# Kernel tuning notes

Measured on AMD Instinct MI355X. Metric: run time of the kernel, lower is better.

The kernel has to match this reference:

```python
import jax, jax.numpy as jnp
import numpy as np

NA, NB = 50000, 50000   # nodes of type A and B
E = 400000              # edges per canonical etype
D = 128                 # embed_size


def setup_inputs() -> dict:
    key = jax.random.key(0)
    ks = jax.random.split(key, 12)
    emb = lambda k, n: jax.random.normal(k, (n, D), dtype=jnp.float32) * 0.05
    return {
        "embed_r0": emb(ks[0], NA),       # srctype A for etype r0 (A->B)
        "embed_r1": emb(ks[1], NB),       # srctype B for etype r1 (B->A)
        "embed_r2": emb(ks[2], NA),       # srctype A for etype r2 (A->A)
        "self_embed_A": emb(ks[3], NA),
        "self_embed_B": emb(ks[4], NB),
        "h_bias": jnp.zeros((D,), jnp.float32),
        "src0": jax.random.randint(ks[5], (E,), 0, NA, dtype=jnp.int32),
        "dst0": jax.random.randint(ks[6], (E,), 0, NB, dtype=jnp.int32),
        "src1": jax.random.randint(ks[7], (E,), 0, NB, dtype=jnp.int32),
        "dst1": jax.random.randint(ks[8], (E,), 0, NA, dtype=jnp.int32),
        "src2": jax.random.randint(ks[9], (E,), 0, NA, dtype=jnp.int32),
        "dst2": jax.random.randint(ks[10], (E,), 0, NA, dtype=jnp.int32),
    }


def _mean_agg(embed, src, dst, n_dst):
    # DGL copy_u + mean: gather source embeds along edges, mean per dst node
    msg = embed[src]                                                   # [E, D]
    summed = jax.ops.segment_sum(msg, dst, num_segments=n_dst)         # [n_dst, D]
    cnt = jax.ops.segment_sum(jnp.ones((src.shape[0],), embed.dtype), dst,
                              num_segments=n_dst)                      # [n_dst]
    return summed / jnp.maximum(cnt, 1.0)[:, None]  # zero-indegree nodes -> 0


def reference(embed_r0, embed_r1, embed_r2, self_embed_A, self_embed_B, h_bias,
              src0, dst0, src1, dst1, src2, dst2):
    # multi_update_all(funcs, 'sum'): per-etype mean, then sum over etypes per dst ntype
    h_B = _mean_agg(embed_r0, src0, dst0, NB)
    h_A = _mean_agg(embed_r1, src1, dst1, NA) + _mean_agg(embed_r2, src2, dst2, NA)
    # fused epilogue: self-loop embed add, bias, activation; dropout p=0 -> identity
    h_A = jax.nn.relu(h_A + self_embed_A + h_bias)
    h_B = jax.nn.relu(h_B + self_embed_B + h_bias)
    return (h_A, h_B)
```

## Files before the change

kernel.cpp:

```cpp
#include <hip/hip_runtime.h>

#define D 128
#define SLOTS 32

typedef float vf4 __attribute__((ext_vector_type(4)));
typedef int   vi2 __attribute__((ext_vector_type(2)));
typedef _Float16 half4 __attribute__((ext_vector_type(4)));
typedef _Float16 half8 __attribute__((ext_vector_type(8)));

__device__ __forceinline__ vf4 nt_load4(const float* p) {
    return __builtin_nontemporal_load(reinterpret_cast<const vf4*>(p));
}
__device__ __forceinline__ void nt_store4(float* p, vf4 v) {
    __builtin_nontemporal_store(v, reinterpret_cast<vf4*>(p));
}
__device__ __forceinline__ vf4 ld4(const float* p) {
    return *reinterpret_cast<const vf4*>(p);
}

__global__ void init_kernel(int* __restrict__ cnt, int nt, int clearBlocks,
                            const float* __restrict__ er1, const float* __restrict__ er2,
                            const float* __restrict__ er0,
                            _Float16* __restrict__ hdst,
                            long long s1, long long s2, long long s0) {
    if (blockIdx.x < clearBlocks) {
        int i = blockIdx.x * blockDim.x + threadIdx.x;
        if (i < nt) cnt[i] = 0;
        return;
    }
    long long t = (long long)(blockIdx.x - clearBlocks) * blockDim.x + threadIdx.x;
    long long f = t * 8;
    long long total = s1 + s2 + s0;
    if (f >= total) return;
    const float* sp; long long off;
    if (f < s1)           { sp = er1; off = f; }
    else if (f < s1 + s2) { sp = er2; off = f - s1; }
    else                  { sp = er0; off = f - s1 - s2; }
    vf4 a = nt_load4(sp + off);
    vf4 b = nt_load4(sp + off + 4);
    half8 h;
    h[0] = (_Float16)a.x; h[1] = (_Float16)a.y; h[2] = (_Float16)a.z; h[3] = (_Float16)a.w;
    h[4] = (_Float16)b.x; h[5] = (_Float16)b.y; h[6] = (_Float16)b.z; h[7] = (_Float16)b.w;
    __builtin_nontemporal_store(h, reinterpret_cast<half8*>(hdst + f));
}

__global__ void build_kernel(const int* __restrict__ src1, const int* __restrict__ dst1, int e1,
                             const int* __restrict__ src2, const int* __restrict__ dst2, int e2,
                             const int* __restrict__ src0, const int* __restrict__ dst0, int e0,
                             int* __restrict__ cnt, unsigned short* __restrict__ slots, int na) {
    int mypart = blockIdx.x & 7;
    int t = (blockIdx.x >> 3) * blockDim.x + threadIdx.x;
    int s, c;
    if (t < e1) {
        s = src1[t];
        c = 2 * dst1[t];
    } else if (t < e1 + e2) {
        int i = t - e1;
        s = src2[i];
        c = 2 * dst2[i] + 1;
    } else if (t < e1 + e2 + e0) {
        int i = t - e1 - e2;
        s = src0[i];
        c = 2 * na + dst0[i];
    } else return;
    if (((c >> 11) & 7) != mypart) return;
    int pos = atomicAdd(&cnt[c], 1);
    if (pos < SLOTS) slots[(size_t)c * SLOTS + pos] = (unsigned short)s;
}


template <bool F16>
__device__ __forceinline__ vf4 ldrow(const void* base, int idx, int col) {
    if constexpr (F16) {
        const _Float16* p = (const _Float16*)base + (size_t)idx * D + col;
        half4 h = *reinterpret_cast<const half4*>(p);
        vf4 r;
        r.x = (float)h[0]; r.y = (float)h[1]; r.z = (float)h[2]; r.w = (float)h[3];
        return r;
    } else {
        return ld4((const float*)base + (size_t)idx * D + col);
    }
}

template <bool F16>
__device__ __forceinline__ void seg_tail(const void* __restrict__ emb,
                                         int idxv, int j, int c, int col, vf4& acc) {
    for (; j + 3 < c; j += 4) {
        int i0 = __shfl(idxv, j + 0, 32), i1 = __shfl(idxv, j + 1, 32);
        int i2 = __shfl(idxv, j + 2, 32), i3 = __shfl(idxv, j + 3, 32);
        vf4 v0 = ldrow<F16>(emb, i0, col);
        vf4 v1 = ldrow<F16>(emb, i1, col);
        vf4 v2 = ldrow<F16>(emb, i2, col);
        vf4 v3 = ldrow<F16>(emb, i3, col);
        acc += (v0 + v1) + (v2 + v3);
    }
    for (; j < c; j++) {
        int s = __shfl(idxv, j, 32);
        acc += ldrow<F16>(emb, s, col);
    }
}

template <bool F16>
__device__ __forceinline__ void seg_dual(const void* __restrict__ ea, int idxa, int ca,
                                         const void* __restrict__ eb, int idxb, int cb,
                                         int col, vf4& sa, vf4& sb) {
    int j = 0;
    int m = (ca < cb) ? ca : cb;
    for (; j + 7 < m; j += 8) {
        int a0 = __shfl(idxa, j + 0, 32), a1 = __shfl(idxa, j + 1, 32);
        int a2 = __shfl(idxa, j + 2, 32), a3 = __shfl(idxa, j + 3, 32);
        int a4 = __shfl(idxa, j + 4, 32), a5 = __shfl(idxa, j + 5, 32);
        int a6 = __shfl(idxa, j + 6, 32), a7 = __shfl(idxa, j + 7, 32);
        int b0 = __shfl(idxb, j + 0, 32), b1 = __shfl(idxb, j + 1, 32);
        int b2 = __shfl(idxb, j + 2, 32), b3 = __shfl(idxb, j + 3, 32);
        int b4 = __shfl(idxb, j + 4, 32), b5 = __shfl(idxb, j + 5, 32);
        int b6 = __shfl(idxb, j + 6, 32), b7 = __shfl(idxb, j + 7, 32);
        vf4 va0 = ldrow<F16>(ea, a0, col);
        vf4 va1 = ldrow<F16>(ea, a1, col);
        vf4 va2 = ldrow<F16>(ea, a2, col);
        vf4 va3 = ldrow<F16>(ea, a3, col);
        vf4 va4 = ldrow<F16>(ea, a4, col);
        vf4 va5 = ldrow<F16>(ea, a5, col);
        vf4 va6 = ldrow<F16>(ea, a6, col);
        vf4 va7 = ldrow<F16>(ea, a7, col);
        vf4 vb0 = ldrow<F16>(eb, b0, col);
        vf4 vb1 = ldrow<F16>(eb, b1, col);
        vf4 vb2 = ldrow<F16>(eb, b2, col);
        vf4 vb3 = ldrow<F16>(eb, b3, col);
        vf4 vb4 = ldrow<F16>(eb, b4, col);
        vf4 vb5 = ldrow<F16>(eb, b5, col);
        vf4 vb6 = ldrow<F16>(eb, b6, col);
        vf4 vb7 = ldrow<F16>(eb, b7, col);
        sa += ((va0 + va1) + (va2 + va3)) + ((va4 + va5) + (va6 + va7));
        sb += ((vb0 + vb1) + (vb2 + vb3)) + ((vb4 + vb5) + (vb6 + vb7));
    }
    for (; j + 3 < m; j += 4) {
        int a0 = __shfl(idxa, j + 0, 32), a1 = __shfl(idxa, j + 1, 32);
        int a2 = __shfl(idxa, j + 2, 32), a3 = __shfl(idxa, j + 3, 32);
        int b0 = __shfl(idxb, j + 0, 32), b1 = __shfl(idxb, j + 1, 32);
        int b2 = __shfl(idxb, j + 2, 32), b3 = __shfl(idxb, j + 3, 32);
        vf4 va0 = ldrow<F16>(ea, a0, col);
        vf4 va1 = ldrow<F16>(ea, a1, col);
        vf4 va2 = ldrow<F16>(ea, a2, col);
        vf4 va3 = ldrow<F16>(ea, a3, col);
        vf4 vb0 = ldrow<F16>(eb, b0, col);
        vf4 vb1 = ldrow<F16>(eb, b1, col);
        vf4 vb2 = ldrow<F16>(eb, b2, col);
        vf4 vb3 = ldrow<F16>(eb, b3, col);
        sa += (va0 + va1) + (va2 + va3);
        sb += (vb0 + vb1) + (vb2 + vb3);
    }
    seg_tail<F16>(ea, idxa, j, ca, col, sa);
    seg_tail<F16>(eb, idxb, j, cb, col, sb);
}

__device__ __forceinline__ vf4 relu4(vf4 v) {
    v.x = fmaxf(v.x, 0.0f); v.y = fmaxf(v.y, 0.0f);
    v.z = fmaxf(v.z, 0.0f); v.w = fmaxf(v.w, 0.0f);
    return v;
}

template <bool F16>
__global__ void gather_kernel(const void* __restrict__ emb1,
                              const void* __restrict__ emb2,
                              const void* __restrict__ emb0,
                              const unsigned short* __restrict__ slots,
                              const int* __restrict__ cnt,
                              const float* __restrict__ selfA,
                              const float* __restrict__ selfB,
                              const float* __restrict__ bias,
                              float* __restrict__ out,
                              int na, int nb) {
    int tid = blockIdx.x * blockDim.x + threadIdx.x;
    int gid = tid >> 5;
    int lane = tid & 31;
    int col = lane * 4;
    int nbg = (nb + 1) >> 1;
    if (gid >= na + nbg) return;
    vf4 b = ld4(bias + col);
    if (gid < na) {
        int r = gid;
        vi2 cc = __builtin_nontemporal_load(reinterpret_cast<const vi2*>(cnt + 2 * r));
        int c1 = min(cc.x, SLOTS);
        int c2 = min(cc.y, SLOTS);
        int idx1 = (lane < c1)
            ? (int)__builtin_nontemporal_load(slots + (size_t)(2 * r) * SLOTS + lane) : 0;
        int idx2 = (lane < c2)
            ? (int)__builtin_nontemporal_load(slots + (size_t)(2 * r + 1) * SLOTS + lane) : 0;
        vf4 s1 = {0.f, 0.f, 0.f, 0.f}, s2 = {0.f, 0.f, 0.f, 0.f};
        seg_dual<F16>(emb1, idx1, c1, emb2, idx2, c2, col, s1, s2);
        float inv1 = (c1 > 0) ? 1.0f / (float)c1 : 0.0f;
        float inv2 = (c2 > 0) ? 1.0f / (float)c2 : 0.0f;
        vf4 sf = nt_load4(selfA + (size_t)r * D + col);
        vf4 rr = relu4(s1 * inv1 + s2 * inv2 + sf + b);
        nt_store4(out + (size_t)r * D + col, rr);
    } else {
        int g = gid - na;
        int ra = 2 * g, rb = 2 * g + 1;
        bool hasB = rb < nb;
        vi2 cc = __builtin_nontemporal_load(
            reinterpret_cast<const vi2*>(cnt + 2 * na + ra));
        int ca = min(cc.x, SLOTS);
        int cb = hasB ? min(cc.y, SLOTS) : 0;
        int idxa = (lane < ca)
            ? (int)__builtin_nontemporal_load(slots + (size_t)(2 * na + ra) * SLOTS + lane) : 0;
        int idxb = (lane < cb)
            ? (int)__builtin_nontemporal_load(slots + (size_t)(2 * na + rb) * SLOTS + lane) : 0;
        vf4 sa = {0.f, 0.f, 0.f, 0.f}, sb = {0.f, 0.f, 0.f, 0.f};
        seg_dual<F16>(emb0, idxa, ca, emb0, idxb, cb, col, sa, sb);
        float inva = (ca > 0) ? 1.0f / (float)ca : 0.0f;
        vf4 sfa = nt_load4(selfB + (size_t)ra * D + col);
        vf4 rra = relu4(sa * inva + sfa + b);
        nt_store4(out + (size_t)(na + ra) * D + col, rra);
        if (hasB) {
            float invb = (cb > 0) ? 1.0f / (float)cb : 0.0f;
            vf4 sfb = nt_load4(selfB + (size_t)rb * D + col);
            vf4 rrb = relu4(sb * invb + sfb + b);
            nt_store4(out + (size_t)(na + rb) * D + col, rrb);
        }
    }
}

extern "C" void kernel_launch(void* const* d_in, const int* in_sizes, int n_in,
                              void* d_out, int out_size, void* d_ws, size_t ws_size,
                              hipStream_t stream) {
    const float* embed_r0 = (const float*)d_in[0];
    const float* embed_r1 = (const float*)d_in[1];
    const float* embed_r2 = (const float*)d_in[2];
    const float* selfA    = (const float*)d_in[3];
    const float* selfB    = (const float*)d_in[4];
    const float* bias     = (const float*)d_in[5];
    const int*   src0     = (const int*)d_in[6];
    const int*   dst0     = (const int*)d_in[7];
    const int*   src1     = (const int*)d_in[8];
    const int*   dst1     = (const int*)d_in[9];
    const int*   src2     = (const int*)d_in[10];
    const int*   dst2     = (const int*)d_in[11];

    const int na = in_sizes[3] / D;
    const int nb = in_sizes[4] / D;
    const int e0 = in_sizes[6];
    const int e1 = in_sizes[8];
    const int e2 = in_sizes[10];
    const int etot = e0 + e1 + e2;
    const int NT = 2 * na + nb;

    float* out = (float*)d_out;

    char* ws   = (char*)d_ws;
    int* cnt   = (int*)ws;
    unsigned short* slots = (unsigned short*)(cnt + NT);
    size_t slotsBytes = (size_t)NT * SLOTS * sizeof(unsigned short);
    _Float16* h16 = (_Float16*)((char*)slots + slotsBytes);

    const long long s1 = (long long)nb * D;
    const long long s2 = (long long)na * D;
    const long long s0 = (long long)na * D;
    const long long cvtN = s1 + s2 + s0;
    size_t needed = (size_t)NT * sizeof(int) + slotsBytes + (size_t)cvtN * sizeof(_Float16);
    const bool useF16 = ws_size >= needed;

    const int T = 256;

    int clearBlocks = (NT + T - 1) / T;
    int cvtBlocks = useF16 ? (int)((cvtN / 8 + T - 1) / T) : 0;
    init_kernel<<<clearBlocks + cvtBlocks, T, 0, stream>>>(
        cnt, NT, clearBlocks, embed_r1, embed_r2, embed_r0, h16, s1, s2, s0);

    int nchunks = (etot + T - 1) / T;
    build_kernel<<<nchunks * 8, T, 0, stream>>>(
        src1, dst1, e1, src2, dst2, e2, src0, dst0, e0, cnt, slots, na);

    int nbg = (nb + 1) >> 1;
    int rows = na + nbg;
    long long gthreads = (long long)rows * 32;
    int gb = (int)((gthreads + T - 1) / T);
    if (useF16) {
        gather_kernel<true><<<gb, T, 0, stream>>>(h16, h16 + s1, h16 + s1 + s2, slots, cnt,
                                                  selfA, selfB, bias, out, na, nb);
    } else {
        gather_kernel<false><<<gb, T, 0, stream>>>(embed_r1, embed_r2, embed_r0, slots, cnt,
                                                   selfA, selfB, bias, out, na, nb);
    }
}
```

Before: 288.4 us.

## Match gather block-to-row mapping to build partitions and use cached metadata loads

The gather kernel now maps blocks so that each of the 8 partitions (blockIdx & 7) handles row stripes of 1024 groups. This mirrors the build kernel's partitioning of counters and slots by (c>>11)&7, presumably so that each XCD reads slot and count data that its own L2 already holds from the build phase. The nontemporal loads on cnt and slots become normal cached loads to exploit that locality, and the build kernel now loads the src index only after the partition filter, skipping reads it would discard. The striped mapping launches some blocks that return immediately and relies on the hardware assigning blocks to XCDs round-robin.

```diff
diff --git a/kernel.cpp b/kernel.cpp
--- a/kernel.cpp
+++ b/kernel.cpp
@@ -50,20 +50,22 @@
                              int* __restrict__ cnt, unsigned short* __restrict__ slots, int na) {
     int mypart = blockIdx.x & 7;
     int t = (blockIdx.x >> 3) * blockDim.x + threadIdx.x;
-    int s, c;
+    const int* __restrict__ sp;
+    int c;
     if (t < e1) {
-        s = src1[t];
         c = 2 * dst1[t];
+        sp = src1 + t;
     } else if (t < e1 + e2) {
         int i = t - e1;
-        s = src2[i];
         c = 2 * dst2[i] + 1;
+        sp = src2 + i;
     } else if (t < e1 + e2 + e0) {
         int i = t - e1 - e2;
-        s = src0[i];
         c = 2 * na + dst0[i];
+        sp = src0 + i;
     } else return;
     if (((c >> 11) & 7) != mypart) return;
+    int s = *sp;
     int pos = atomicAdd(&cnt[c], 1);
     if (pos < SLOTS) slots[(size_t)c * SLOTS + pos] = (unsigned short)s;
 }
@@ -171,22 +173,23 @@
                               const float* __restrict__ bias,
                               float* __restrict__ out,
                               int na, int nb) {
-    int tid = blockIdx.x * blockDim.x + threadIdx.x;
-    int gid = tid >> 5;
-    int lane = tid & 31;
+    int q = blockIdx.x & 7;
+    int idx = (blockIdx.x >> 3) * (blockDim.x >> 5) + (threadIdx.x >> 5);
+    int stripe = idx >> 10;
+    int within = idx & 1023;
+    int gid = (((stripe << 3) + q) << 10) + within;
+    int lane = threadIdx.x & 31;
     int col = lane * 4;
     int nbg = (nb + 1) >> 1;
     if (gid >= na + nbg) return;
     vf4 b = ld4(bias + col);
     if (gid < na) {
         int r = gid;
-        vi2 cc = __builtin_nontemporal_load(reinterpret_cast<const vi2*>(cnt + 2 * r));
+        vi2 cc = *reinterpret_cast<const vi2*>(cnt + 2 * r);
         int c1 = min(cc.x, SLOTS);
         int c2 = min(cc.y, SLOTS);
-        int idx1 = (lane < c1)
-            ? (int)__builtin_nontemporal_load(slots + (size_t)(2 * r) * SLOTS + lane) : 0;
-        int idx2 = (lane < c2)
-            ? (int)__builtin_nontemporal_load(slots + (size_t)(2 * r + 1) * SLOTS + lane) : 0;
+        int idx1 = (lane < c1) ? (int)slots[(size_t)(2 * r) * SLOTS + lane] : 0;
+        int idx2 = (lane < c2) ? (int)slots[(size_t)(2 * r + 1) * SLOTS + lane] : 0;
         vf4 s1 = {0.f, 0.f, 0.f, 0.f}, s2 = {0.f, 0.f, 0.f, 0.f};
         seg_dual<F16>(emb1, idx1, c1, emb2, idx2, c2, col, s1, s2);
         float inv1 = (c1 > 0) ? 1.0f / (float)c1 : 0.0f;
@@ -198,14 +201,11 @@
         int g = gid - na;
         int ra = 2 * g, rb = 2 * g + 1;
         bool hasB = rb < nb;
-        vi2 cc = __builtin_nontemporal_load(
-            reinterpret_cast<const vi2*>(cnt + 2 * na + ra));
+        vi2 cc = *reinterpret_cast<const vi2*>(cnt + 2 * na + ra);
         int ca = min(cc.x, SLOTS);
         int cb = hasB ? min(cc.y, SLOTS) : 0;
-        int idxa = (lane < ca)
-            ? (int)__builtin_nontemporal_load(slots + (size_t)(2 * na + ra) * SLOTS + lane) : 0;
-        int idxb = (lane < cb)
-            ? (int)__builtin_nontemporal_load(slots + (size_t)(2 * na + rb) * SLOTS + lane) : 0;
+        int idxa = (lane < ca) ? (int)slots[(size_t)(2 * na + ra) * SLOTS + lane] : 0;
+        int idxb = (lane < cb) ? (int)slots[(size_t)(2 * na + rb) * SLOTS + lane] : 0;
         vf4 sa = {0.f, 0.f, 0.f, 0.f}, sb = {0.f, 0.f, 0.f, 0.f};
         seg_dual<F16>(emb0, idxa, ca, emb0, idxb, cb, col, sa, sb);
         float inva = (ca > 0) ? 1.0f / (float)ca : 0.0f;
@@ -272,9 +272,10 @@
         src1, dst1, e1, src2, dst2, e2, src0, dst0, e0, cnt, slots, na);
 
     int nbg = (nb + 1) >> 1;
-    int rows = na + nbg;
-    long long gthreads = (long long)rows * 32;
-    int gb = (int)((gthreads + T - 1) / T);
+    int ngroups = na + nbg;
+    int stripes = (ngroups + 1023) >> 10;
+    int maxStripesPerPart = (stripes + 7) >> 3;
+    int gb = 8 * maxStripesPerPart * 128;
     if (useF16) {
         gather_kernel<true><<<gb, T, 0, stream>>>(h16, h16 + s1, h16 + s1 + s2, slots, cnt,
                                                   selfA, selfB, bias, out, na, nb);
```

Result: slower. 295.0 us (+2.3%).
